# Performance work log

Measured on AMD Instinct MI355X. Metric: run time of the kernel, lower is better.

Reference implementation:

```python
import jax, jax.numpy as jnp
import numpy as np

B, T, D = 8, 2048, 1024
DK, DV = 1024, 1024


def setup_inputs() -> dict:
    key = jax.random.key(0)
    ks = jax.random.split(key, 7)
    s = 1.0 / np.sqrt(D)
    return {
        "X": jax.random.normal(ks[0], (B, T, D), dtype=jnp.float32),
        "Wq": jax.random.uniform(ks[1], (D, DK), jnp.float32, -s, s),
        "bq": jax.random.uniform(ks[2], (DK,), jnp.float32, -s, s),
        "Wk": jax.random.uniform(ks[3], (D, DK), jnp.float32, -s, s),
        "bk": jax.random.uniform(ks[4], (DK,), jnp.float32, -s, s),
        "Wv": jax.random.uniform(ks[5], (D, DV), jnp.float32, -s, s),
        "bv": jax.random.uniform(ks[6], (DV,), jnp.float32, -s, s),
    }


def reference(X, Wq, bq, Wk, bk, Wv, bv):
    # relu-activated projections (note: original applies relu to Q, K, V; no 1/sqrt(d) scaling)
    Q = jax.nn.relu(jnp.einsum("btd,dk->btk", X, Wq) + bq)  # [B,T,DK]
    K = jax.nn.relu(jnp.einsum("btd,dk->btk", X, Wk) + bk)  # [B,T,DK]
    V = jax.nn.relu(jnp.einsum("btd,dv->btv", X, Wv) + bv)  # [B,T,DV]
    scores = jnp.einsum("btk,bsk->bts", Q, K)               # [B,T,S] query t attends over keys s
    attn = jax.nn.softmax(scores, axis=-1)
    return jnp.einsum("bts,bsv->btv", attn, V)              # [B,T,DV]
```

## Files before the change

### kernel.cpp

```cpp
#include <hip/hip_runtime.h>

typedef __bf16 bf16x8 __attribute__((ext_vector_type(8)));
typedef _Float16 f16x8 __attribute__((ext_vector_type(8)));
typedef float floatx4 __attribute__((ext_vector_type(4)));

__device__ __forceinline__ unsigned short f2bf(float f) {
  unsigned int u = __float_as_uint(f);
  u += 0x7FFFu + ((u >> 16) & 1u);
  return (unsigned short)(u >> 16);
}
__device__ __forceinline__ unsigned short f2h(float f) {
  _Float16 h = (_Float16)f;
  return __builtin_bit_cast(unsigned short, h);
}
template <bool F16>
__device__ __forceinline__ unsigned short f2x(float f) {
  return F16 ? f2h(f) : f2bf(f);
}

__device__ __forceinline__ void g2l16(const void* g, void* l) {
  __builtin_amdgcn_global_load_lds(
      (const __attribute__((address_space(1))) void*)g,
      (__attribute__((address_space(3))) void*)l, 16, 0, 0);
}

template <int MODE, bool AF32, bool INF16, bool OUTF16, int SWM>
__global__ __launch_bounds__(256) void gemm_bt(
    const void* __restrict__ Av, int lda, long sA,
    const unsigned short* __restrict__ B, int ldb, long sB,
    void* __restrict__ Cv, int ldc, long sC,
    int K, const float* __restrict__ bias, float* __restrict__ lrow) {
  __shared__ unsigned short As[128 * 64];
  __shared__ unsigned short Bs[128 * 64];
  const int tid = threadIdx.x;
  const int wave = tid >> 6, lane = tid & 63;
  const int z = blockIdx.z;
  const unsigned short* A16 = (const unsigned short*)Av + (size_t)z * sA;
  const float* A32 = (const float*)Av + (size_t)z * sA;
  B += (size_t)z * sB;
  const int m0 = blockIdx.y * 128, n0 = blockIdx.x * 128;
  const int wr = (wave >> 1) * 64;
  const int wc = (wave & 1) * 64;
  const int qr = lane >> 4, lr = lane & 15;
  floatx4 acc[4][4] = {};

  for (int k0 = 0; k0 < K; k0 += 64) {
    __syncthreads();
    if (AF32) {
#pragma unroll
      for (int it = 0; it < 8; ++it) {
        const int idx = it * 256 + tid;
        const int row = idx >> 4, c4 = idx & 15;
        float4 v = *(const float4*)(A32 + (size_t)(m0 + row) * lda + k0 + c4 * 4);
        const int soff = (((c4 >> 1) ^ (row & SWM)) * 2 + (c4 & 1)) * 4;
        *(ushort4*)&As[row * 64 + soff] =
            make_ushort4(f2x<INF16>(v.x), f2x<INF16>(v.y),
                         f2x<INF16>(v.z), f2x<INF16>(v.w));
      }
    } else {
#pragma unroll
      for (int it = 0; it < 4; ++it) {
        const int base = it * 256 + wave * 64;
        const int idx = base + lane;
        const int row = idx >> 3;
        const int gs = (idx & 7) ^ (row & SWM);
        g2l16(A16 + (size_t)(m0 + row) * lda + k0 + gs * 8, &As[base * 8]);
      }
    }
#pragma unroll
    for (int it = 0; it < 4; ++it) {
      const int base = it * 256 + wave * 64;
      const int idx = base + lane;
      const int row = idx >> 3;
      const int gs = (idx & 7) ^ (row & SWM);
      g2l16(B + (size_t)(n0 + row) * ldb + k0 + gs * 8, &Bs[base * 8]);
    }
    __syncthreads();
#pragma unroll
    for (int kk = 0; kk < 64; kk += 32) {
      const int t = (kk >> 3) + qr;
      if (INF16) {
        f16x8 af[4], bf[4];
#pragma unroll
        for (int i = 0; i < 4; ++i) {
          const int ra = wr + i * 16 + lr;
          af[i] = *(const f16x8*)&As[ra * 64 + ((t ^ (ra & SWM)) * 8)];
        }
#pragma unroll
        for (int j = 0; j < 4; ++j) {
          const int rb = wc + j * 16 + lr;
          bf[j] = *(const f16x8*)&Bs[rb * 64 + ((t ^ (rb & SWM)) * 8)];
        }
#pragma unroll
        for (int i = 0; i < 4; ++i)
#pragma unroll
          for (int j = 0; j < 4; ++j)
            acc[i][j] = __builtin_amdgcn_mfma_f32_16x16x32_f16(bf[j], af[i],
                                                               acc[i][j], 0, 0, 0);
      } else {
        bf16x8 af[4], bf[4];
#pragma unroll
        for (int i = 0; i < 4; ++i) {
          const int ra = wr + i * 16 + lr;
          af[i] = *(const bf16x8*)&As[ra * 64 + ((t ^ (ra & SWM)) * 8)];
        }
#pragma unroll
        for (int j = 0; j < 4; ++j) {
          const int rb = wc + j * 16 + lr;
          bf[j] = *(const bf16x8*)&Bs[rb * 64 + ((t ^ (rb & SWM)) * 8)];
        }
#pragma unroll
        for (int i = 0; i < 4; ++i)
#pragma unroll
          for (int j = 0; j < 4; ++j)
            acc[i][j] = __builtin_amdgcn_mfma_f32_16x16x32_bf16(bf[j], af[i],
                                                                acc[i][j], 0, 0, 0);
      }
    }
  }

  float* Cf = (float*)Cv + (size_t)z * sC;
  unsigned short* Cb = (unsigned short*)Cv + (size_t)z * sC;
#pragma unroll
  for (int i = 0; i < 4; ++i) {
    const int row = m0 + wr + i * 16 + lr;
    float rowsum = 0.0f;
    float invl = 1.0f;
    if (MODE == 2) invl = 1.0f / lrow[(size_t)z * 2048 + row];
#pragma unroll
    for (int j = 0; j < 4; ++j) {
      const int col0 = n0 + wc + j * 16 + qr * 4;
      if (MODE == 0) {
        float4 bj = *(const float4*)(bias + col0);
        float v0 = fmaxf(acc[i][j][0] + bj.x, 0.0f);
        float v1 = fmaxf(acc[i][j][1] + bj.y, 0.0f);
        float v2 = fmaxf(acc[i][j][2] + bj.z, 0.0f);
        float v3 = fmaxf(acc[i][j][3] + bj.w, 0.0f);
        *(ushort4*)&Cb[(size_t)row * ldc + col0] =
            make_ushort4(f2x<OUTF16>(v0), f2x<OUTF16>(v1),
                         f2x<OUTF16>(v2), f2x<OUTF16>(v3));
      } else if (MODE == 1) {
        float e0 = __expf(acc[i][j][0] - 60.0f);
        float e1 = __expf(acc[i][j][1] - 60.0f);
        float e2 = __expf(acc[i][j][2] - 60.0f);
        float e3 = __expf(acc[i][j][3] - 60.0f);
        *(ushort4*)&Cb[(size_t)row * ldc + col0] =
            make_ushort4(f2bf(e0), f2bf(e1), f2bf(e2), f2bf(e3));
        rowsum += (e0 + e1) + (e2 + e3);
      } else {
        *(float4*)&Cf[(size_t)row * ldc + col0] =
            make_float4(acc[i][j][0] * invl, acc[i][j][1] * invl,
                        acc[i][j][2] * invl, acc[i][j][3] * invl);
      }
    }
    if (MODE == 1) {
      rowsum += __shfl_xor(rowsum, 16);
      rowsum += __shfl_xor(rowsum, 32);
      if (lane < 16)
        atomicAdd(&lrow[(size_t)z * 2048 + row], rowsum);
    }
  }
}

template <bool F16>
__global__ __launch_bounds__(256) void cvt16(const float* __restrict__ in,
                                             unsigned short* __restrict__ out,
                                             int n) {
  const int i = (blockIdx.x * 256 + threadIdx.x) * 8;
  if (i >= n) return;
  float4 a = *(const float4*)(in + i);
  float4 b = *(const float4*)(in + i + 4);
  *(ushort4*)(out + i) =
      make_ushort4(f2x<F16>(a.x), f2x<F16>(a.y), f2x<F16>(a.z), f2x<F16>(a.w));
  *(ushort4*)(out + i + 4) =
      make_ushort4(f2x<F16>(b.x), f2x<F16>(b.y), f2x<F16>(b.z), f2x<F16>(b.w));
}

template <bool F16>
__global__ __launch_bounds__(256) void wtrans(const float* __restrict__ W,
                                              unsigned short* __restrict__ Wt) {
  __shared__ unsigned short t[64][68];
  const int tid = threadIdx.x;
  const int n0 = blockIdx.x * 64, k0 = blockIdx.y * 64;
#pragma unroll
  for (int it = 0; it < 4; ++it) {
    const int idx = it * 256 + tid;
    const int kr = idx >> 4, nq = idx & 15;
    float4 v = *(const float4*)&W[(size_t)(k0 + kr) * 1024 + n0 + nq * 4];
    t[kr][nq * 4 + 0] = f2x<F16>(v.x);
    t[kr][nq * 4 + 1] = f2x<F16>(v.y);
    t[kr][nq * 4 + 2] = f2x<F16>(v.z);
    t[kr][nq * 4 + 3] = f2x<F16>(v.w);
  }
  __syncthreads();
#pragma unroll
  for (int it = 0; it < 4; ++it) {
    const int idx = it * 256 + tid;
    const int nr = idx >> 4, kq = idx & 15;
    *(ushort4*)&Wt[(size_t)(n0 + nr) * 1024 + k0 + kq * 4] =
        make_ushort4(t[kq * 4 + 0][nr], t[kq * 4 + 1][nr],
                     t[kq * 4 + 2][nr], t[kq * 4 + 3][nr]);
  }
}

__global__ __launch_bounds__(256) void vtrans(const unsigned short* __restrict__ V,
                                              unsigned short* __restrict__ Vt) {
  __shared__ unsigned short t[64][68];
  const int tid = threadIdx.x;
  const int v0 = blockIdx.x * 64, t0 = blockIdx.y * 64;
  const int b = blockIdx.z;
  const unsigned short* Vb = V + (size_t)b * 2048 * 1024;
  unsigned short* Vtb = Vt + (size_t)b * 1024 * 2048;
#pragma unroll
  for (int it = 0; it < 4; ++it) {
    const int idx = it * 256 + tid;
    const int tr = idx >> 4, vq = idx & 15;
    ushort4 u = *(const ushort4*)&Vb[(size_t)(t0 + tr) * 1024 + v0 + vq * 4];
    t[tr][vq * 4 + 0] = u.x;
    t[tr][vq * 4 + 1] = u.y;
    t[tr][vq * 4 + 2] = u.z;
    t[tr][vq * 4 + 3] = u.w;
  }
  __syncthreads();
#pragma unroll
  for (int it = 0; it < 4; ++it) {
    const int idx = it * 256 + tid;
    const int vr = idx >> 4, tq = idx & 15;
    *(ushort4*)&Vtb[(size_t)(v0 + vr) * 2048 + t0 + tq * 4] =
        make_ushort4(t[tq * 4 + 0][vr], t[tq * 4 + 1][vr],
                     t[tq * 4 + 2][vr], t[tq * 4 + 3][vr]);
  }
}

__global__ void zero_f32(float* __restrict__ p, int n) {
  const int i = blockIdx.x * 256 + threadIdx.x;
  if (i < n) p[i] = 0.0f;
}

__global__ __launch_bounds__(256) void copy_half(const float* __restrict__ T,
                                                 float* __restrict__ out,
                                                 int roff) {
  const size_t i = ((size_t)blockIdx.x * 256 + threadIdx.x) * 4;
  const size_t b = i >> 20;
  const size_t rem = i & 1048575;
  float4 v = *(const float4*)(T + i);
  *(float4*)(out + b * 2097152 + (size_t)roff * 1024 + rem) = v;
}

__global__ void diag_ws(float* __restrict__ out, float mb) { out[0] = mb; }

extern "C" void kernel_launch(void* const* d_in, const int* in_sizes, int n_in,
                              void* d_out, int out_size, void* d_ws, size_t ws_size,
                              hipStream_t stream) {
  const float* X = (const float*)d_in[0];
  const float* Wq = (const float*)d_in[1];
  const float* bq = (const float*)d_in[2];
  const float* Wk = (const float*)d_in[3];
  const float* bk = (const float*)d_in[4];
  const float* Wv = (const float*)d_in[5];
  const float* bv = (const float*)d_in[6];
  float* out = (float*)d_out;
  char* ws = (char*)d_ws;
  const size_t MiB = 1ull << 20;

  const size_t B_WQT = 0, B_WKT = 2 * MiB, B_WVT = 4 * MiB;
  const size_t B_Q = 6 * MiB;
  const size_t B_K = 38 * MiB;
  const size_t B_E = 70 * MiB;
  const size_t B_L = 134 * MiB;
  const size_t NEEDED_BIG = B_L + 65536;

  const size_t S_WQT = 0, S_WKT = 2 * MiB, S_WVT = 4 * MiB;
  const size_t S_Q = 6 * MiB, S_K = 38 * MiB, S_L = 70 * MiB;
  const size_t NEEDED_SMALL = S_L + 65536;

  if (ws_size >= NEEDED_BIG) {
    unsigned short* Wqt = (unsigned short*)(ws + B_WQT);
    unsigned short* Wkt = (unsigned short*)(ws + B_WKT);
    unsigned short* Wvt = (unsigned short*)(ws + B_WVT);
    unsigned short* Q   = (unsigned short*)(ws + B_Q);
    unsigned short* Kb  = (unsigned short*)(ws + B_K);
    unsigned short* E   = (unsigned short*)(ws + B_E);
    float* l            = (float*)(ws + B_L);
    unsigned short* Xh = (unsigned short*)d_out;
    unsigned short* V  = (unsigned short*)d_out + 16384ull * 1024;

    cvt16<true><<<8192, 256, 0, stream>>>(X, Xh, 16384 * 1024);
    wtrans<true><<<dim3(16, 16), 256, 0, stream>>>(Wq, Wqt);
    wtrans<true><<<dim3(16, 16), 256, 0, stream>>>(Wk, Wkt);
    wtrans<true><<<dim3(16, 16), 256, 0, stream>>>(Wv, Wvt);
    zero_f32<<<64, 256, 0, stream>>>(l, 16384);

    gemm_bt<0, false, true, true, 0><<<dim3(8, 128, 1), 256, 0, stream>>>(
        Xh, 1024, 0, Wqt, 1024, 0, Q, 1024, 0, 1024, bq, nullptr);
    gemm_bt<0, false, true, true, 7><<<dim3(8, 128, 1), 256, 0, stream>>>(
        Xh, 1024, 0, Wkt, 1024, 0, Kb, 1024, 0, 1024, bk, nullptr);
    gemm_bt<0, false, true, false, 7><<<dim3(8, 128, 1), 256, 0, stream>>>(
        Xh, 1024, 0, Wvt, 1024, 0, V, 1024, 0, 1024, bv, nullptr);

    gemm_bt<1, false, true, false, 7><<<dim3(16, 16, 8), 256, 0, stream>>>(
        Q, 1024, 2048L * 1024, Kb, 1024, 2048L * 1024,
        E, 2048, 2048L * 2048, 1024, nullptr, l);

    vtrans<<<dim3(16, 32, 8), 256, 0, stream>>>(V, Q);

    gemm_bt<2, false, false, false, 7><<<dim3(8, 16, 8), 256, 0, stream>>>(
        E, 2048, 2048L * 2048, Q, 2048, 1024L * 2048,
        out, 1024, 2048L * 1024, 2048, nullptr, l);
    return;
  }

  if (ws_size < NEEDED_SMALL) {
    diag_ws<<<1, 1, 0, stream>>>(out, (float)(ws_size >> 20));
    return;
  }

  unsigned short* Wqt = (unsigned short*)(ws + S_WQT);
  unsigned short* Wkt = (unsigned short*)(ws + S_WKT);
  unsigned short* Wvt = (unsigned short*)(ws + S_WVT);
  unsigned short* Q   = (unsigned short*)(ws + S_Q);
  unsigned short* Kb  = (unsigned short*)(ws + S_K);
  float* l            = (float*)(ws + S_L);
  unsigned short* Xh = (unsigned short*)d_out;
  unsigned short* E  = (unsigned short*)d_out;

  cvt16<true><<<8192, 256, 0, stream>>>(X, Xh, 16384 * 1024);
  wtrans<true><<<dim3(16, 16), 256, 0, stream>>>(Wq, Wqt);
  wtrans<true><<<dim3(16, 16), 256, 0, stream>>>(Wk, Wkt);
  wtrans<true><<<dim3(16, 16), 256, 0, stream>>>(Wv, Wvt);
  zero_f32<<<64, 256, 0, stream>>>(l, 16384);

  gemm_bt<0, false, true, true, 0><<<dim3(8, 128, 1), 256, 0, stream>>>(
      Xh, 1024, 0, Wqt, 1024, 0, Q, 1024, 0, 1024, bq, nullptr);
  gemm_bt<0, false, true, true, 7><<<dim3(8, 128, 1), 256, 0, stream>>>(
      Xh, 1024, 0, Wkt, 1024, 0, Kb, 1024, 0, 1024, bk, nullptr);

  gemm_bt<1, false, true, false, 7><<<dim3(16, 16, 8), 256, 0, stream>>>(
      Q, 1024, 2048L * 1024, Kb, 1024, 2048L * 1024,
      E, 2048, 2048L * 2048, 1024, nullptr, l);

  gemm_bt<0, true, true, false, 7><<<dim3(8, 128, 1), 256, 0, stream>>>(
      X, 1024, 0, Wvt, 1024, 0, Kb, 1024, 0, 1024, bv, nullptr);

  vtrans<<<dim3(16, 32, 8), 256, 0, stream>>>(Kb, Q);

  float* T = (float*)Kb;
  gemm_bt<2, false, false, false, 7><<<dim3(8, 8, 8), 256, 0, stream>>>(
      E, 2048, 2048L * 2048, Q, 2048, 1024L * 2048,
      T, 1024, 1024L * 1024, 2048, nullptr, l);
  copy_half<<<8192, 256, 0, stream>>>(T, out, 0);
  gemm_bt<2, false, false, false, 7><<<dim3(8, 8, 8), 256, 0, stream>>>(
      E + 1024L * 2048, 2048, 2048L * 2048, Q, 2048, 1024L * 2048,
      T, 1024, 1024L * 1024, 2048, nullptr, l + 1024);
  copy_half<<<8192, 256, 0, stream>>>(T, out, 1024);
}
```

Baseline: 491.7 us.

## Double-buffer LDS tiles with async prefetch and XCD-aware block remap in GEMM

Gives the shared GEMM kernel ping-pong LDS buffers for A and B. The next K tile is issued with global_load_lds before computing the current one, and explicit vmcnt waits plus raw barriers replace the two syncthreads per iteration. Blocks are also remapped so consecutive flat ids spread across 8 groups, likely to improve L2 locality per XCD, and the LDS swizzle is fixed to 7 for all GEMMs (it was 0 for the Q projection). Doubling LDS to 64KB per block may reduce occupancy.

```diff
diff --git a/kernel.cpp b/kernel.cpp
--- a/kernel.cpp
+++ b/kernel.cpp
@@ -24,98 +24,144 @@
       (__attribute__((address_space(3))) void*)l, 16, 0, 0);
 }
 
-template <int MODE, bool AF32, bool INF16, bool OUTF16, int SWM>
+template <int MODE, bool AF32, bool INF16, bool OUTF16>
 __global__ __launch_bounds__(256) void gemm_bt(
     const void* __restrict__ Av, int lda, long sA,
     const unsigned short* __restrict__ B, int ldb, long sB,
     void* __restrict__ Cv, int ldc, long sC,
     int K, const float* __restrict__ bias, float* __restrict__ lrow) {
-  __shared__ unsigned short As[128 * 64];
-  __shared__ unsigned short Bs[128 * 64];
+  __shared__ unsigned short As[2][128 * 64];
+  __shared__ unsigned short Bs[2][128 * 64];
   const int tid = threadIdx.x;
   const int wave = tid >> 6, lane = tid & 63;
   const int z = blockIdx.z;
   const unsigned short* A16 = (const unsigned short*)Av + (size_t)z * sA;
   const float* A32 = (const float*)Av + (size_t)z * sA;
   B += (size_t)z * sB;
-  const int m0 = blockIdx.y * 128, n0 = blockIdx.x * 128;
+
+  int bx = blockIdx.x, by = blockIdx.y;
+  {
+    const int nwg = gridDim.x * gridDim.y;
+    if ((nwg & 7) == 0) {
+      int flat = by * gridDim.x + bx;
+      flat = (flat & 7) * (nwg >> 3) + (flat >> 3);
+      bx = flat % gridDim.x;
+      by = flat / gridDim.x;
+    }
+  }
+  const int m0 = by * 128, n0 = bx * 128;
   const int wr = (wave >> 1) * 64;
   const int wc = (wave & 1) * 64;
   const int qr = lane >> 4, lr = lane & 15;
   floatx4 acc[4][4] = {};
 
-  for (int k0 = 0; k0 < K; k0 += 64) {
-    __syncthreads();
-    if (AF32) {
+  auto stageAB = [&](int t, int buf) {
+    const int k0 = t << 6;
+#pragma unroll
+    for (int it = 0; it < 4; ++it) {
+      const int base = it * 256 + wave * 64;
+      const int idx = base + lane;
+      const int row = idx >> 3;
+      const int gs = (idx & 7) ^ (row & 7);
+      g2l16(A16 + (size_t)(m0 + row) * lda + k0 + gs * 8, &As[buf][base * 8]);
+    }
+#pragma unroll
+    for (int it = 0; it < 4; ++it) {
+      const int base = it * 256 + wave * 64;
+      const int idx = base + lane;
+      const int row = idx >> 3;
+      const int gs = (idx & 7) ^ (row & 7);
+      g2l16(B + (size_t)(n0 + row) * ldb + k0 + gs * 8, &Bs[buf][base * 8]);
+    }
+  };
+
+  auto computeT = [&](int buf) {
+#pragma unroll
+    for (int kk = 0; kk < 64; kk += 32) {
+      const int slot = (kk >> 3) + qr;
+      if (INF16) {
+        f16x8 af[4], bf[4];
+#pragma unroll
+        for (int i = 0; i < 4; ++i) {
+          const int ra = wr + i * 16 + lr;
+          af[i] = *(const f16x8*)&As[buf][ra * 64 + ((slot ^ (ra & 7)) * 8)];
+        }
+#pragma unroll
+        for (int j = 0; j < 4; ++j) {
+          const int rb = wc + j * 16 + lr;
+          bf[j] = *(const f16x8*)&Bs[buf][rb * 64 + ((slot ^ (rb & 7)) * 8)];
+        }
+#pragma unroll
+        for (int i = 0; i < 4; ++i)
+#pragma unroll
+          for (int j = 0; j < 4; ++j)
+            acc[i][j] = __builtin_amdgcn_mfma_f32_16x16x32_f16(
+                bf[j], af[i], acc[i][j], 0, 0, 0);
+      } else {
+        bf16x8 af[4], bf[4];
+#pragma unroll
+        for (int i = 0; i < 4; ++i) {
+          const int ra = wr + i * 16 + lr;
+          af[i] = *(const bf16x8*)&As[buf][ra * 64 + ((slot ^ (ra & 7)) * 8)];
+        }
+#pragma unroll
+        for (int j = 0; j < 4; ++j) {
+          const int rb = wc + j * 16 + lr;
+          bf[j] = *(const bf16x8*)&Bs[buf][rb * 64 + ((slot ^ (rb & 7)) * 8)];
+        }
+#pragma unroll
+        for (int i = 0; i < 4; ++i)
+#pragma unroll
+          for (int j = 0; j < 4; ++j)
+            acc[i][j] = __builtin_amdgcn_mfma_f32_16x16x32_bf16(
+                bf[j], af[i], acc[i][j], 0, 0, 0);
+      }
+    }
+  };
+
+  if (!AF32) {
+    const int nk = K >> 6;
+    stageAB(0, 0);
+    for (int t = 0; t < nk; ++t) {
+      const int cur = t & 1;
+      if (t + 1 < nk) {
+        stageAB(t + 1, cur ^ 1);
+        asm volatile("s_waitcnt vmcnt(8)" ::: "memory");
+      } else {
+        asm volatile("s_waitcnt vmcnt(0)" ::: "memory");
+      }
+      __builtin_amdgcn_sched_barrier(0);
+      __builtin_amdgcn_s_barrier();
+      __builtin_amdgcn_sched_barrier(0);
+      computeT(cur);
+      __builtin_amdgcn_sched_barrier(0);
+      __builtin_amdgcn_s_barrier();
+      __builtin_amdgcn_sched_barrier(0);
+    }
+  } else {
+    for (int k0 = 0; k0 < K; k0 += 64) {
+      __syncthreads();
 #pragma unroll
       for (int it = 0; it < 8; ++it) {
         const int idx = it * 256 + tid;
         const int row = idx >> 4, c4 = idx & 15;
-        float4 v = *(const float4*)(A32 + (size_t)(m0 + row) * lda + k0 + c4 * 4);
-        const int soff = (((c4 >> 1) ^ (row & SWM)) * 2 + (c4 & 1)) * 4;
-        *(ushort4*)&As[row * 64 + soff] =
-            make_ushort4(f2x<INF16>(v.x), f2x<INF16>(v.y),
-                         f2x<INF16>(v.z), f2x<INF16>(v.w));
+        float4 v =
+            *(const float4*)(A32 + (size_t)(m0 + row) * lda + k0 + c4 * 4);
+        const int soff = (((c4 >> 1) ^ (row & 7)) * 2 + (c4 & 1)) * 4;
+        *(ushort4*)&As[0][row * 64 + soff] =
+            make_ushort4(f2x<INF16>(v.x), f2x<INF16>(v.y), f2x<INF16>(v.z),
+                         f2x<INF16>(v.w));
       }
-    } else {
 #pragma unroll
       for (int it = 0; it < 4; ++it) {
         const int base = it * 256 + wave * 64;
         const int idx = base + lane;
         const int row = idx >> 3;
-        const int gs = (idx & 7) ^ (row & SWM);
-        g2l16(A16 + (size_t)(m0 + row) * lda + k0 + gs * 8, &As[base * 8]);
+        const int gs = (idx & 7) ^ (row & 7);
+        g2l16(B + (size_t)(n0 + row) * ldb + k0 + gs * 8, &Bs[0][base * 8]);
       }
-    }
-#pragma unroll
-    for (int it = 0; it < 4; ++it) {
-      const int base = it * 256 + wave * 64;
-      const int idx = base + lane;
-      const int row = idx >> 3;
-      const int gs = (idx & 7) ^ (row & SWM);
-      g2l16(B + (size_t)(n0 + row) * ldb + k0 + gs * 8, &Bs[base * 8]);
-    }
-    __syncthreads();
-#pragma unroll
-    for (int kk = 0; kk < 64; kk += 32) {
-      const int t = (kk >> 3) + qr;
-      if (INF16) {
-        f16x8 af[4], bf[4];
-#pragma unroll
-        for (int i = 0; i < 4; ++i) {
-          const int ra = wr + i * 16 + lr;
-          af[i] = *(const f16x8*)&As[ra * 64 + ((t ^ (ra & SWM)) * 8)];
-        }
-#pragma unroll
-        for (int j = 0; j < 4; ++j) {
-          const int rb = wc + j * 16 + lr;
-          bf[j] = *(const f16x8*)&Bs[rb * 64 + ((t ^ (rb & SWM)) * 8)];
-        }
-#pragma unroll
-        for (int i = 0; i < 4; ++i)
-#pragma unroll
-          for (int j = 0; j < 4; ++j)
-            acc[i][j] = __builtin_amdgcn_mfma_f32_16x16x32_f16(bf[j], af[i],
-                                                               acc[i][j], 0, 0, 0);
-      } else {
-        bf16x8 af[4], bf[4];
-#pragma unroll
-        for (int i = 0; i < 4; ++i) {
-          const int ra = wr + i * 16 + lr;
-          af[i] = *(const bf16x8*)&As[ra * 64 + ((t ^ (ra & SWM)) * 8)];
-        }
-#pragma unroll
-        for (int j = 0; j < 4; ++j) {
-          const int rb = wc + j * 16 + lr;
-          bf[j] = *(const bf16x8*)&Bs[rb * 64 + ((t ^ (rb & SWM)) * 8)];
-        }
-#pragma unroll
-        for (int i = 0; i < 4; ++i)
-#pragma unroll
-          for (int j = 0; j < 4; ++j)
-            acc[i][j] = __builtin_amdgcn_mfma_f32_16x16x32_bf16(bf[j], af[i],
-                                                                acc[i][j], 0, 0, 0);
-      }
+      __syncthreads();
+      computeT(0);
     }
   }
 
@@ -137,8 +183,8 @@
         float v2 = fmaxf(acc[i][j][2] + bj.z, 0.0f);
         float v3 = fmaxf(acc[i][j][3] + bj.w, 0.0f);
         *(ushort4*)&Cb[(size_t)row * ldc + col0] =
-            make_ushort4(f2x<OUTF16>(v0), f2x<OUTF16>(v1),
-                         f2x<OUTF16>(v2), f2x<OUTF16>(v3));
+            make_ushort4(f2x<OUTF16>(v0), f2x<OUTF16>(v1), f2x<OUTF16>(v2),
+                         f2x<OUTF16>(v3));
       } else if (MODE == 1) {
         float e0 = __expf(acc[i][j][0] - 60.0f);
         float e1 = __expf(acc[i][j][1] - 60.0f);
@@ -291,20 +337,20 @@
     wtrans<true><<<dim3(16, 16), 256, 0, stream>>>(Wv, Wvt);
     zero_f32<<<64, 256, 0, stream>>>(l, 16384);
 
-    gemm_bt<0, false, true, true, 0><<<dim3(8, 128, 1), 256, 0, stream>>>(
+    gemm_bt<0, false, true, true><<<dim3(8, 128, 1), 256, 0, stream>>>(
         Xh, 1024, 0, Wqt, 1024, 0, Q, 1024, 0, 1024, bq, nullptr);
-    gemm_bt<0, false, true, true, 7><<<dim3(8, 128, 1), 256, 0, stream>>>(
+    gemm_bt<0, false, true, true><<<dim3(8, 128, 1), 256, 0, stream>>>(
         Xh, 1024, 0, Wkt, 1024, 0, Kb, 1024, 0, 1024, bk, nullptr);
-    gemm_bt<0, false, true, false, 7><<<dim3(8, 128, 1), 256, 0, stream>>>(
+    gemm_bt<0, false, true, false><<<dim3(8, 128, 1), 256, 0, stream>>>(
         Xh, 1024, 0, Wvt, 1024, 0, V, 1024, 0, 1024, bv, nullptr);
 
-    gemm_bt<1, false, true, false, 7><<<dim3(16, 16, 8), 256, 0, stream>>>(
+    gemm_bt<1, false, true, false><<<dim3(16, 16, 8), 256, 0, stream>>>(
         Q, 1024, 2048L * 1024, Kb, 1024, 2048L * 1024,
         E, 2048, 2048L * 2048, 1024, nullptr, l);
 
     vtrans<<<dim3(16, 32, 8), 256, 0, stream>>>(V, Q);
 
-    gemm_bt<2, false, false, false, 7><<<dim3(8, 16, 8), 256, 0, stream>>>(
+    gemm_bt<2, false, false, false><<<dim3(8, 16, 8), 256, 0, stream>>>(
         E, 2048, 2048L * 2048, Q, 2048, 1024L * 2048,
         out, 1024, 2048L * 1024, 2048, nullptr, l);
     return;
@@ -330,26 +376,26 @@
   wtrans<true><<<dim3(16, 16), 256, 0, stream>>>(Wv, Wvt);
   zero_f32<<<64, 256, 0, stream>>>(l, 16384);
 
-  gemm_bt<0, false, true, true, 0><<<dim3(8, 128, 1), 256, 0, stream>>>(
+  gemm_bt<0, false, true, true><<<dim3(8, 128, 1), 256, 0, stream>>>(
       Xh, 1024, 0, Wqt, 1024, 0, Q, 1024, 0, 1024, bq, nullptr);
-  gemm_bt<0, false, true, true, 7><<<dim3(8, 128, 1), 256, 0, stream>>>(
+  gemm_bt<0, false, true, true><<<dim3(8, 128, 1), 256, 0, stream>>>(
       Xh, 1024, 0, Wkt, 1024, 0, Kb, 1024, 0, 1024, bk, nullptr);
 
-  gemm_bt<1, false, true, false, 7><<<dim3(16, 16, 8), 256, 0, stream>>>(
+  gemm_bt<1, false, true, false><<<dim3(16, 16, 8), 256, 0, stream>>>(
       Q, 1024, 2048L * 1024, Kb, 1024, 2048L * 1024,
       E, 2048, 2048L * 2048, 1024, nullptr, l);
 
-  gemm_bt<0, true, true, false, 7><<<dim3(8, 128, 1), 256, 0, stream>>>(
+  gemm_bt<0, true, true, false><<<dim3(8, 128, 1), 256, 0, stream>>>(
       X, 1024, 0, Wvt, 1024, 0, Kb, 1024, 0, 1024, bv, nullptr);
 
   vtrans<<<dim3(16, 32, 8), 256, 0, stream>>>(Kb, Q);
 
   float* T = (float*)Kb;
-  gemm_bt<2, false, false, false, 7><<<dim3(8, 8, 8), 256, 0, stream>>>(
+  gemm_bt<2, false, false, false><<<dim3(8, 8, 8), 256, 0, stream>>>(
       E, 2048, 2048L * 2048, Q, 2048, 1024L * 2048,
       T, 1024, 1024L * 1024, 2048, nullptr, l);
   copy_half<<<8192, 256, 0, stream>>>(T, out, 0);
-  gemm_bt<2, false, false, false, 7><<<dim3(8, 8, 8), 256, 0, stream>>>(
+  gemm_bt<2, false, false, false><<<dim3(8, 8, 8), 256, 0, stream>>>(
       E + 1024L * 2048, 2048, 2048L * 2048, Q, 2048, 1024L * 2048,
       T, 1024, 1024L * 1024, 2048, nullptr, l + 1024);
   copy_half<<<8192, 256, 0, stream>>>(T, out, 1024);
```

Result: faster. 443.4 us (-9.8%).
